# Kernel tuning notes

Hardware: AMD Instinct MI355X
Metric: run time of the kernel (lower is better)

## Reference

```python
import jax, jax.numpy as jnp
import numpy as np

T, K, F = 131072, 64, 8
EPS = 1e-10


def setup_inputs() -> dict:
    key = jax.random.key(0)
    k0, k1, k2, k3 = jax.random.split(key, 4)
    return {
        "observations": jax.random.normal(k0, (T, F), dtype=jnp.float32),
        "beta_logits": jax.random.normal(k1, (K,), dtype=jnp.float32),
        "pi_logits": jax.random.normal(k2, (K, K), dtype=jnp.float32),
        "means": 0.1 * jax.random.normal(k3, (K, F), dtype=jnp.float32),
        "log_vars": jnp.zeros((K, F), dtype=jnp.float32),
    }


def _stick_breaking(logits):
    betas = jax.nn.sigmoid(logits)
    cp = jnp.cumprod(1.0 - betas)
    return betas * jnp.concatenate([jnp.ones((1,), betas.dtype), cp[:-1]])


def _emission_log_probs(obs, means, log_vars):
    # Diagonal-covariance MVN log-prob, vectorized over (T, K) via matmuls
    # logN(x; mu, diag(v)) = -0.5 * (sum((x-mu)^2/v) + sum(log v) + F*log(2pi))
    inv_var = jnp.exp(-log_vars)                                 # (K, F)
    quad = (obs ** 2) @ inv_var.T                                # (T, K): sum x^2/v
    cross = obs @ (means * inv_var).T                            # (T, K): sum x*mu/v
    const = jnp.sum(means ** 2 * inv_var + log_vars, axis=1)     # (K,)
    log2pi = jnp.float32(np.log(2.0 * np.pi))
    Fdim = obs.shape[1]
    return -0.5 * (quad - 2.0 * cross + const[None, :] + Fdim * log2pi)


def reference(observations, beta_logits, pi_logits, means, log_vars):
    beta_w = _stick_breaking(beta_logits)                        # (K,)
    trans = jax.nn.softmax(pi_logits, axis=1)                    # (K, K)
    em = jnp.exp(_emission_log_probs(observations, means, log_vars))  # (T, K)

    # Forward recursion
    a0 = beta_w * em[0]
    a0 = a0 / (a0.sum() + EPS)

    def fwd_step(a, e):
        a = (a @ trans) * e
        a = a / (a.sum() + EPS)
        return a, a

    _, alpha_rest = jax.lax.scan(fwd_step, a0, em[1:])
    alpha = jnp.concatenate([a0[None, :], alpha_rest], axis=0)   # (T, K)

    # Backward recursion: beta[t] = normalize(trans @ (beta[t+1] * em[t+1]))
    bT = jnp.ones((trans.shape[0],), observations.dtype)

    def bwd_step(b, e_next):
        b = trans @ (b * e_next)
        b = b / (b.sum() + EPS)
        return b, b

    _, beta_rev = jax.lax.scan(bwd_step, bT, em[1:], reverse=True)
    beta = jnp.concatenate([beta_rev, bT[None, :]], axis=0)      # (T, K)

    log_likelihood = jnp.log(alpha[-1].sum() + EPS)
    return alpha, beta, log_likelihood
```

## Files before the change

### kernel.cpp

```cpp
#include <hip/hip_runtime.h>

#define T_N   131072
#define K_N   64
#define L_C   128
#define F_N   8
#define N_CH  (T_N / L_C)
#define WARM  96
#define EPS_F 1e-10f
#define OBS_MAX ((T_N - 1) * F_N)

#define LOG2E 1.4426950408889634f
#define NL2E  (-0.72134752044448170f)
#define LN2   0.6931471805599453f
#define LN2PI 1.8378770664093453f
#define EMSC  16.0f

typedef float v2f __attribute__((ext_vector_type(2)));
typedef __attribute__((ext_vector_type(4))) float f32x4;

template <int CTRL>
__device__ __forceinline__ float dpp_add(float x) {
  int y = __builtin_amdgcn_update_dpp(0, __float_as_int(x), CTRL, 0xF, 0xF, true);
  return x + __int_as_float(y);
}
__device__ __forceinline__ float wave_sum64(float x) {
  x = dpp_add<0x111>(x);
  x = dpp_add<0x112>(x);
  x = dpp_add<0x114>(x);
  x = dpp_add<0x118>(x);
  x = dpp_add<0x142>(x);
  x = dpp_add<0x143>(x);
  return __int_as_float(__builtin_amdgcn_readlane(__float_as_int(x), 63));
}

#define PKFMA(a, b, c) __builtin_elementwise_fma(a, b, c)

__device__ __forceinline__ float em_pk(const float4& xa, const float4& xb,
                                       const v2f civ2[4], const v2f cmiv2[4],
                                       float cc) {
  v2f x0 = {xa.x, xa.y}, x1 = {xa.z, xa.w};
  v2f x2 = {xb.x, xb.y}, x3 = {xb.z, xb.w};
  v2f a0 = {cc, 0.f}, a1 = {0.f, 0.f};
  a0 = PKFMA(x0, PKFMA(x0, civ2[0], cmiv2[0]), a0);
  a1 = PKFMA(x1, PKFMA(x1, civ2[1], cmiv2[1]), a1);
  a0 = PKFMA(x2, PKFMA(x2, civ2[2], cmiv2[2]), a0);
  a1 = PKFMA(x3, PKFMA(x3, civ2[3], cmiv2[3]), a1);
  v2f s = a0 + a1;
  return __builtin_amdgcn_exp2f(s.x + s.y);
}

#define MATVEC(VV, MOUT)                                                      \
  {                                                                           \
    vtab[lane] = (VV);                                                        \
    v2f ac0_ = {0.f, 0.f}, ac1_ = {0.f, 0.f};                                 \
    v2f ac2_ = {0.f, 0.f}, ac3_ = {0.f, 0.f};                                 \
    _Pragma("unroll")                                                         \
    for (int r_ = 0; r_ < 16; ++r_) {                                         \
      f32x4 q_ = ((const f32x4*)vtab)[r_];                                    \
      v2f lo_ = __builtin_shufflevector(q_, q_, 0, 1);                        \
      v2f hi_ = __builtin_shufflevector(q_, q_, 2, 3);                        \
      if (r_ & 1) {                                                           \
        ac2_ = PKFMA(lo_, Tc[2 * r_],     ac2_);                              \
        ac3_ = PKFMA(hi_, Tc[2 * r_ + 1], ac3_);                              \
      } else {                                                                \
        ac0_ = PKFMA(lo_, Tc[2 * r_],     ac0_);                              \
        ac1_ = PKFMA(hi_, Tc[2 * r_ + 1], ac1_);                              \
      }                                                                       \
    }                                                                         \
    v2f s0_ = ac0_ + ac1_, s1_ = ac2_ + ac3_;                                 \
    v2f s2_ = s0_ + s1_;                                                      \
    MOUT = s2_.x + s2_.y;                                                     \
  }

extern "C" __global__ void __launch_bounds__(64, 2)
hdphmm_fb(const float* __restrict__ obs,
          const float* __restrict__ beta_logits,
          const float* __restrict__ pi_logits,
          const float* __restrict__ means,
          const float* __restrict__ log_vars,
          float* __restrict__ out) {
  const int lane = threadIdx.x;
  const int bid  = blockIdx.x;

  __shared__ __align__(8) float2 sstat[K_N];
  __shared__ float sb[K_N];
  __shared__ __align__(16) float vtab[K_N];

  float* alpha   = out;
  float* betaout = out + (size_t)T_N * K_N;

  v2f civ2[4], cmiv2[4];
  float c0, cw;
  {
    const float4* mp = reinterpret_cast<const float4*>(means + lane * F_N);
    const float4* lp = reinterpret_cast<const float4*>(log_vars + lane * F_N);
    float4 m0 = mp[0], m1 = mp[1];
    float4 l0 = lp[0], l1 = lp[1];
    float mu[8] = {m0.x, m0.y, m0.z, m0.w, m1.x, m1.y, m1.z, m1.w};
    float lv[8] = {l0.x, l0.y, l0.z, l0.w, l1.x, l1.y, l1.z, l1.w};
    float cst = F_N * LN2PI;
#pragma unroll
    for (int f = 0; f < 8; ++f) {
      float iv = __builtin_amdgcn_exp2f(-lv[f] * LOG2E);
      cst += lv[f] + mu[f] * mu[f] * iv;
      float cf  = NL2E * iv;
      civ2[f >> 1][f & 1]  = cf;
      cmiv2[f >> 1][f & 1] = -2.0f * mu[f] * cf;
    }
    c0 = NL2E * cst;
    cw = c0 + EMSC;
  }

  {
    const float4* pr4 = reinterpret_cast<const float4*>(pi_logits + lane * K_N);
    float mx = -3.0e38f;
#pragma unroll
    for (int k = 0; k < 16; ++k) {
      float4 r = pr4[k];
      mx = fmaxf(mx, fmaxf(fmaxf(r.x, r.y), fmaxf(r.z, r.w)));
    }
    float s = 0.0f;
#pragma unroll
    for (int k = 0; k < 16; ++k) {
      float4 r = pr4[k];
      s += __builtin_amdgcn_exp2f((r.x - mx) * LOG2E);
      s += __builtin_amdgcn_exp2f((r.y - mx) * LOG2E);
      s += __builtin_amdgcn_exp2f((r.z - mx) * LOG2E);
      s += __builtin_amdgcn_exp2f((r.w - mx) * LOG2E);
    }
    sstat[lane] = make_float2(mx, __builtin_amdgcn_rcpf(s));
  }
  __syncthreads();

  v2f Tc[32];

  if (bid < N_CH) {
#pragma unroll
    for (int j = 0; j < 32; ++j) {
      float2 sa = sstat[2 * j];
      float2 sbv = sstat[2 * j + 1];
      float p0 = pi_logits[(size_t)(2 * j) * K_N + lane];
      float p1 = pi_logits[(size_t)(2 * j + 1) * K_N + lane];
      Tc[j] = (v2f){__builtin_amdgcn_exp2f((p0 - sa.x) * LOG2E) * sa.y,
                    __builtin_amdgcn_exp2f((p1 - sbv.x) * LOG2E) * sbv.y};
    }

    const int out_lo = bid * L_C;
    float v;
    int t_first;
    if (bid == 0) {
      float bl = beta_logits[lane];
      float ex = __builtin_amdgcn_exp2f(-bl * LOG2E);
      float bw = __builtin_amdgcn_rcpf(1.0f + ex);
      sb[lane] = 1.0f - bw;
      __syncthreads();
      float pr = 1.0f;
#pragma unroll
      for (int i = 0; i < 64; ++i) {
        float qv = sb[i];
        pr = (i < lane) ? pr * qv : pr;
      }
      float4 x0 = reinterpret_cast<const float4*>(obs)[0];
      float4 x1 = reinterpret_cast<const float4*>(obs)[1];
      v = bw * pr * em_pk(x0, x1, civ2, cmiv2, c0);
      t_first = 1;
    } else {
      const int t0 = out_lo - WARM;
      const float4* xp = reinterpret_cast<const float4*>(obs + t0 * F_N);
      v = em_pk(xp[0], xp[1], civ2, cmiv2, cw);
      t_first = t0 + 1;
    }
    int obs_off = t_first * F_N;
    float4 xa, xb;
    {
      const float4* xp = reinterpret_cast<const float4*>(obs + obs_off);
      xa = xp[0]; xb = xp[1];
    }
    int out_off = out_lo * K_N + lane;

    const int wn8 = (bid == 0) ? 0 : (WARM >> 3);
#pragma unroll 1
    for (int o = 0; o < wn8; ++o) {
#pragma unroll
      for (int i = 0; i < 8; ++i) {
        float4 nxa = *reinterpret_cast<const float4*>(obs + obs_off + F_N);
        float4 nxb = *reinterpret_cast<const float4*>(obs + obs_off + F_N + 4);
        float m;
        MATVEC(v, m)
        float e = em_pk(xa, xb, civ2, cmiv2, cw);
        v = m * e;
        xa = nxa; xb = nxb; obs_off += F_N;
      }
      float Sw = wave_sum64(v);
      v *= __builtin_amdgcn_rcpf(Sw);
    }

    float S = wave_sum64(v);
    float r_st = __builtin_amdgcn_rcpf(S + EPS_F);

#define FWD_SSTEP                                                             \
  {                                                                           \
    int offn = obs_off + F_N; offn = (offn > OBS_MAX) ? OBS_MAX : offn;       \
    float4 nxa = *reinterpret_cast<const float4*>(obs + offn);                \
    float4 nxb = *reinterpret_cast<const float4*>(obs + offn + 4);            \
    float m;                                                                  \
    MATVEC(v, m)                                                              \
    alpha[out_off] = v * r_st; out_off += K_N;                                \
    float e = em_pk(xa, xb, civ2, cmiv2, c0);                                 \
    float vn = m * (r_st * e);                                                \
    S = wave_sum64(vn);                                                       \
    r_st = __builtin_amdgcn_rcpf(S + EPS_F);                                  \
    v = vn; xa = nxa; xb = nxb; obs_off = offn;                               \
  }

#pragma unroll 2
    for (int it = 0; it < L_C - 1; ++it) FWD_SSTEP
#undef FWD_SSTEP
    alpha[out_off] = v * r_st;
    if (bid == N_CH - 1 && lane == 0) {
      float sl = S * r_st + EPS_F;
      out[(size_t)2 * T_N * K_N] = __builtin_amdgcn_logf(sl) * LN2;
    }
  } else {
    {
      float2 st = sstat[lane];
      const float4* pr4 = reinterpret_cast<const float4*>(pi_logits + lane * K_N);
#pragma unroll
      for (int j2 = 0; j2 < 16; ++j2) {
        float4 r = pr4[j2];
        Tc[2 * j2] = (v2f){__builtin_amdgcn_exp2f((r.x - st.x) * LOG2E) * st.y,
                           __builtin_amdgcn_exp2f((r.y - st.x) * LOG2E) * st.y};
        Tc[2 * j2 + 1] =
            (v2f){__builtin_amdgcn_exp2f((r.z - st.x) * LOG2E) * st.y,
                  __builtin_amdgcn_exp2f((r.w - st.x) * LOG2E) * st.y};
      }
    }

    const int cb   = bid - N_CH;
    const int t_lo = cb * L_C;
    const int t_hi = t_lo + L_C - 1;
    int t_top = t_hi + WARM;
    if (t_top > T_N - 1) t_top = T_N - 1;
    const int s_top = (cb == N_CH - 1) ? T_N - 2 : t_hi;

    float w;
    {
      const float4* xp = reinterpret_cast<const float4*>(obs + t_top * F_N);
      w = em_pk(xp[0], xp[1], civ2, cmiv2, cw);
    }
    if (cb == N_CH - 1)
      betaout[(size_t)(T_N - 1) * K_N + lane] = 1.0f;
    int obs_off = (t_top - 1) * F_N;
    float4 xa, xb;
    {
      const float4* xp = reinterpret_cast<const float4*>(obs + obs_off);
      xa = xp[0]; xb = xp[1];
    }
    int out_off = s_top * K_N + lane;

#define BWD_WSTEP                                                             \
  {                                                                           \
    float4 nxa = *reinterpret_cast<const float4*>(obs + obs_off - F_N);       \
    float4 nxb = *reinterpret_cast<const float4*>(obs + obs_off - F_N + 4);   \
    float m;                                                                  \
    MATVEC(w, m)                                                              \
    float e = em_pk(xa, xb, civ2, cmiv2, cw);                                 \
    w = m * e;                                                                \
    xa = nxa; xb = nxb; obs_off -= F_N;                                       \
  }

    const int pw  = (t_top - s_top) - 1;
    const int pw8 = pw >> 3, pwr = pw & 7;
#pragma unroll 1
    for (int o = 0; o < pw8; ++o) {
#pragma unroll
      for (int i = 0; i < 8; ++i) BWD_WSTEP
      float Sw = wave_sum64(w);
      w *= __builtin_amdgcn_rcpf(Sw);
    }
#pragma unroll 1
    for (int it = 0; it < pwr; ++it) BWD_WSTEP
#undef BWD_WSTEP

    float u, S, r_st;
    {
      float m;
      MATVEC(w, m)
      float Sm = wave_sum64(m);
      u = m * __builtin_amdgcn_rcpf(Sm);
      float e = em_pk(xa, xb, civ2, cmiv2, c0);
      w = u * e;
      S = wave_sum64(u);
      r_st = __builtin_amdgcn_rcpf(S + EPS_F);
      int offn = obs_off - F_N; offn = (offn < 0) ? 0 : offn;
      xa = *reinterpret_cast<const float4*>(obs + offn);
      xb = *reinterpret_cast<const float4*>(obs + offn + 4);
      obs_off = offn;
    }

#define BWD_SSTEP                                                             \
  {                                                                           \
    int offn = obs_off - F_N; offn = (offn < 0) ? 0 : offn;                   \
    float4 nxa = *reinterpret_cast<const float4*>(obs + offn);                \
    float4 nxb = *reinterpret_cast<const float4*>(obs + offn + 4);            \
    float m;                                                                  \
    MATVEC(w, m)                                                              \
    betaout[out_off] = u * r_st; out_off -= K_N;                              \
    float u2 = m * r_st;                                                      \
    float e = em_pk(xa, xb, civ2, cmiv2, c0);                                 \
    w = u2 * e;                                                               \
    S = wave_sum64(u2);                                                       \
    r_st = __builtin_amdgcn_rcpf(S + EPS_F);                                  \
    u = u2; xa = nxa; xb = nxb; obs_off = offn;                               \
  }

    const int store_n = s_top - t_lo;
#pragma unroll 2
    for (int it = 0; it < store_n; ++it) BWD_SSTEP
#undef BWD_SSTEP
    betaout[t_lo * K_N + lane] = u * r_st;
  }
}

extern "C" void kernel_launch(void* const* d_in, const int* in_sizes, int n_in,
                              void* d_out, int out_size, void* d_ws, size_t ws_size,
                              hipStream_t stream) {
  (void)in_sizes; (void)n_in; (void)out_size; (void)d_ws; (void)ws_size;
  const float* obs  = (const float*)d_in[0];
  const float* bl   = (const float*)d_in[1];
  const float* pi   = (const float*)d_in[2];
  const float* mns  = (const float*)d_in[3];
  const float* lvs  = (const float*)d_in[4];
  hipLaunchKernelGGL(hdphmm_fb, dim3(2 * N_CH), dim3(64), 0, stream,
                     obs, bl, pi, mns, lvs, (float*)d_out);
}
```

Baseline: 172.3 us.

## Split the 64x64 matvec across lane quarters and combine partials with cross-lane permutes

Each step's transition matvec used to have every lane read all 64 entries of the shared state vector from LDS (16 b128 loads) and accumulate its full output column. Now each lane reads only the 16-entry quarter belonging to its 16-lane group (4 b128 loads). It computes partial dot products for four output columns (lane^0, lane^16, lane^32, lane^48) using a transition matrix held in registers in a re-permuted layout. The four partials are combined with one ds_swizzle and two ds_bpermute exchanges. This cuts LDS read traffic and latency on the serial critical path, at the cost of extra cross-lane permute latency and a more complex register layout of the transition matrix.

```diff
diff --git a/kernel.cpp b/kernel.cpp
--- a/kernel.cpp
+++ b/kernel.cpp
@@ -52,24 +52,37 @@
 #define MATVEC(VV, MOUT)                                                      \
   {                                                                           \
     vtab[lane] = (VV);                                                        \
-    v2f ac0_ = {0.f, 0.f}, ac1_ = {0.f, 0.f};                                 \
-    v2f ac2_ = {0.f, 0.f}, ac3_ = {0.f, 0.f};                                 \
+    f32x4 q0_ = vq[0], q1_ = vq[1], q2_ = vq[2], q3_ = vq[3];                 \
+    v2f q0l_ = {q0_.x, q0_.y}, q0h_ = {q0_.z, q0_.w};                         \
+    v2f q1l_ = {q1_.x, q1_.y}, q1h_ = {q1_.z, q1_.w};                         \
+    v2f q2l_ = {q2_.x, q2_.y}, q2h_ = {q2_.z, q2_.w};                         \
+    v2f q3l_ = {q3_.x, q3_.y}, q3h_ = {q3_.z, q3_.w};                         \
+    float X0_, X1_, X2_, X3_;                                                 \
     _Pragma("unroll")                                                         \
-    for (int r_ = 0; r_ < 16; ++r_) {                                         \
-      f32x4 q_ = ((const f32x4*)vtab)[r_];                                    \
-      v2f lo_ = __builtin_shufflevector(q_, q_, 0, 1);                        \
-      v2f hi_ = __builtin_shufflevector(q_, q_, 2, 3);                        \
-      if (r_ & 1) {                                                           \
-        ac2_ = PKFMA(lo_, Tc[2 * r_],     ac2_);                              \
-        ac3_ = PKFMA(hi_, Tc[2 * r_ + 1], ac3_);                              \
-      } else {                                                                \
-        ac0_ = PKFMA(lo_, Tc[2 * r_],     ac0_);                              \
-        ac1_ = PKFMA(hi_, Tc[2 * r_ + 1], ac1_);                              \
-      }                                                                       \
+    for (int d_ = 0; d_ < 4; ++d_) {                                          \
+      v2f aA_ = {0.f, 0.f}, aB_ = {0.f, 0.f};                                 \
+      aA_ = PKFMA(q0l_, Tq[d_][0], aA_);                                      \
+      aB_ = PKFMA(q0h_, Tq[d_][1], aB_);                                      \
+      aA_ = PKFMA(q1l_, Tq[d_][2], aA_);                                      \
+      aB_ = PKFMA(q1h_, Tq[d_][3], aB_);                                      \
+      aA_ = PKFMA(q2l_, Tq[d_][4], aA_);                                      \
+      aB_ = PKFMA(q2h_, Tq[d_][5], aB_);                                      \
+      aA_ = PKFMA(q3l_, Tq[d_][6], aA_);                                      \
+      aB_ = PKFMA(q3h_, Tq[d_][7], aB_);                                      \
+      v2f s_ = aA_ + aB_;                                                     \
+      float xs_ = s_.x + s_.y;                                                \
+      if (d_ == 0) X0_ = xs_;                                                 \
+      else if (d_ == 1) X1_ = xs_;                                            \
+      else if (d_ == 2) X2_ = xs_;                                            \
+      else X3_ = xs_;                                                         \
     }                                                                         \
-    v2f s0_ = ac0_ + ac1_, s1_ = ac2_ + ac3_;                                 \
-    v2f s2_ = s0_ + s1_;                                                      \
-    MOUT = s2_.x + s2_.y;                                                     \
+    float e1_ = __int_as_float(                                               \
+        __builtin_amdgcn_ds_swizzle(__float_as_int(X1_), 0x401F));            \
+    float e2_ = __int_as_float(                                               \
+        __builtin_amdgcn_ds_bpermute(a32, __float_as_int(X2_)));              \
+    float e3_ = __int_as_float(                                               \
+        __builtin_amdgcn_ds_bpermute(a48, __float_as_int(X3_)));              \
+    MOUT = (X0_ + e1_) + (e2_ + e3_);                                         \
   }
 
 extern "C" __global__ void __launch_bounds__(64, 2)
@@ -81,10 +94,14 @@
           float* __restrict__ out) {
   const int lane = threadIdx.x;
   const int bid  = blockIdx.x;
+  const int g16  = (lane >> 4) << 4;
+  const int a32  = ((lane ^ 32) & 63) << 2;
+  const int a48  = ((lane ^ 48) & 63) << 2;
 
   __shared__ __align__(8) float2 sstat[K_N];
   __shared__ float sb[K_N];
   __shared__ __align__(16) float vtab[K_N];
+  const f32x4* vq = reinterpret_cast<const f32x4*>(vtab) + (lane >> 4) * 4;
 
   float* alpha   = out;
   float* betaout = out + (size_t)T_N * K_N;
@@ -132,17 +149,21 @@
   }
   __syncthreads();
 
-  v2f Tc[32];
+  v2f Tq[4][8];
 
   if (bid < N_CH) {
 #pragma unroll
-    for (int j = 0; j < 32; ++j) {
-      float2 sa = sstat[2 * j];
-      float2 sbv = sstat[2 * j + 1];
-      float p0 = pi_logits[(size_t)(2 * j) * K_N + lane];
-      float p1 = pi_logits[(size_t)(2 * j + 1) * K_N + lane];
-      Tc[j] = (v2f){__builtin_amdgcn_exp2f((p0 - sa.x) * LOG2E) * sa.y,
-                    __builtin_amdgcn_exp2f((p1 - sbv.x) * LOG2E) * sbv.y};
+    for (int d = 0; d < 4; ++d) {
+      int row = lane ^ (16 * d);
+#pragma unroll
+      for (int c = 0; c < 8; ++c) {
+        int k0 = g16 + 2 * c, k1 = k0 + 1;
+        float2 s0 = sstat[k0], s1 = sstat[k1];
+        float p0 = pi_logits[(size_t)k0 * K_N + row];
+        float p1 = pi_logits[(size_t)k1 * K_N + row];
+        Tq[d][c] = (v2f){__builtin_amdgcn_exp2f((p0 - s0.x) * LOG2E) * s0.y,
+                         __builtin_amdgcn_exp2f((p1 - s1.x) * LOG2E) * s1.y};
+      }
     }
 
     const int out_lo = bid * L_C;
@@ -222,15 +243,19 @@
       out[(size_t)2 * T_N * K_N] = __builtin_amdgcn_logf(sl) * LN2;
     }
   } else {
-    {
-      float2 st = sstat[lane];
-      const float4* pr4 = reinterpret_cast<const float4*>(pi_logits + lane * K_N);
-#pragma unroll
-      for (int j2 = 0; j2 < 16; ++j2) {
-        float4 r = pr4[j2];
-        Tc[2 * j2] = (v2f){__builtin_amdgcn_exp2f((r.x - st.x) * LOG2E) * st.y,
-                           __builtin_amdgcn_exp2f((r.y - st.x) * LOG2E) * st.y};
-        Tc[2 * j2 + 1] =
+#pragma unroll
+    for (int d = 0; d < 4; ++d) {
+      int row = lane ^ (16 * d);
+      float2 st = sstat[row];
+      const float4* rp =
+          reinterpret_cast<const float4*>(pi_logits + (size_t)row * K_N + g16);
+#pragma unroll
+      for (int c4 = 0; c4 < 4; ++c4) {
+        float4 r = rp[c4];
+        Tq[d][2 * c4] =
+            (v2f){__builtin_amdgcn_exp2f((r.x - st.x) * LOG2E) * st.y,
+                  __builtin_amdgcn_exp2f((r.y - st.x) * LOG2E) * st.y};
+        Tq[d][2 * c4 + 1] =
             (v2f){__builtin_amdgcn_exp2f((r.z - st.x) * LOG2E) * st.y,
                   __builtin_amdgcn_exp2f((r.w - st.x) * LOG2E) * st.y};
       }
```

New measurement: 164.4 us. 1.05x faster.
